# Kernel optimization log

Measured on AMD Instinct MI355X. Metric: run time of the kernel, lower is better.

Reference implementation:

```python
import jax, jax.numpy as jnp
import numpy as np

NUM_HEADS = 4
GROUPS = 8          # min(8, ch) with ch=256
EPS = 1e-5          # torch GroupNorm default eps


def setup_inputs() -> dict:
    key = jax.random.key(0)
    ks = jax.random.split(key, 3)
    b, c, h, w = 8, 256, 32, 32
    x = jax.random.normal(ks[0], (b, c, h, w), jnp.float32)
    gn_gamma = jnp.ones((c,), jnp.float32)
    gn_beta = jnp.zeros((c,), jnp.float32)
    qkv_w = jax.random.normal(ks[1], (3 * c, c), jnp.float32) * (c ** -0.5)
    qkv_b = jnp.zeros((3 * c,), jnp.float32)
    proj_w = jax.random.normal(ks[2], (c, c), jnp.float32) * (c ** -0.5)
    proj_b = jnp.zeros((c,), jnp.float32)
    return {"x": x, "gn_gamma": gn_gamma, "gn_beta": gn_beta,
            "qkv_w": qkv_w, "qkv_b": qkv_b, "proj_w": proj_w, "proj_b": proj_b}


def _group_norm(x, gamma, beta):
    b, c, h, w = x.shape
    xg = x.reshape(b, GROUPS, c // GROUPS, h, w)
    mean = xg.mean(axis=(2, 3, 4), keepdims=True)
    var = xg.var(axis=(2, 3, 4), keepdims=True)
    xn = ((xg - mean) * jax.lax.rsqrt(var + EPS)).reshape(b, c, h, w)
    return xn * gamma[None, :, None, None] + beta[None, :, None, None]


def reference(x, gn_gamma, gn_beta, qkv_w, qkv_b, proj_w, proj_b):
    b, c, h, w = x.shape
    dh = c // NUM_HEADS
    xn = _group_norm(x, gn_gamma, gn_beta)
    # 1x1 conv == channel matmul
    qkv = jnp.einsum('oc,bchw->bohw', qkv_w, xn) + qkv_b[None, :, None, None]
    qkv = qkv.reshape(b, 3, NUM_HEADS, dh, h * w)
    q, k, v = qkv[:, 0], qkv[:, 1], qkv[:, 2]   # each (b, n, dh, hw)
    scale = dh ** -0.5
    # full (hw x hw) attention matrix, matching the original explicit einsum
    attn = jax.nn.softmax(jnp.einsum('bncd,bnce->bnde', q, k) * scale, axis=-1)
    out = jnp.einsum('bnde,bnce->bncd', attn, v).reshape(b, c, h, w)
    out = jnp.einsum('oc,bchw->bohw', proj_w, out) + proj_b[None, :, None, None]
    return x + out
```

## Files before the change

### kernel.cpp

```cpp
#include <hip/hip_runtime.h>
#include <stdint.h>

typedef __attribute__((ext_vector_type(8))) short short8;
typedef __attribute__((ext_vector_type(4))) float f32x4;
typedef __attribute__((ext_vector_type(16))) float f32x16;
typedef unsigned long long u64;

#define BB 8
#define CC 256
#define PP 1024
#define NH 4
#define DH 64

#define QSCALE 0.18033688f

__device__ __forceinline__ unsigned short f2bf(float f) {
  union { float f; unsigned u; } v; v.f = f;
  unsigned r = v.u + 0x7FFFu + ((v.u >> 16) & 1u);
  return (unsigned short)(r >> 16);
}

__device__ __forceinline__ f32x4 mfma16(short8 a, short8 b, f32x4 c) {
  return __builtin_amdgcn_mfma_f32_16x16x32_bf16(a, b, c, 0, 0, 0);
}
__device__ __forceinline__ f32x16 mfma32(short8 a, short8 b, f32x16 c) {
  return __builtin_amdgcn_mfma_f32_32x32x16_bf16(a, b, c, 0, 0, 0);
}

__global__ __launch_bounds__(256) void prep(
    const float* __restrict__ x, float2* __restrict__ part,
    const float* __restrict__ qkvw, const float* __restrict__ projw,
    unsigned short* __restrict__ wall) {
  int blk = blockIdx.x;
  int tid = threadIdx.x;
  if (blk < 512) {
    int sl = blk & 7, g = (blk >> 3) & 7, b = blk >> 6;
    const float4* xb =
        (const float4*)(x + (size_t)(b * CC + g * 32) * PP) + sl * 1024;
    float s = 0.f, q = 0.f;
    for (int i = tid; i < 1024; i += 256) {
      float4 v = xb[i];
      s += v.x + v.y + v.z + v.w;
      q += v.x * v.x + v.y * v.y + v.z * v.z + v.w * v.w;
    }
    for (int off = 32; off > 0; off >>= 1) {
      s += __shfl_down(s, off);
      q += __shfl_down(q, off);
    }
    __shared__ float rs[4], rq[4];
    int w = tid >> 6;
    if ((tid & 63) == 0) { rs[w] = s; rq[w] = q; }
    __syncthreads();
    if (tid == 0)
      part[blk] = make_float2(rs[0] + rs[1] + rs[2] + rs[3],
                              rq[0] + rq[1] + rq[2] + rq[3]);
  } else {
    int i4 = (blk - 512) * 256 + tid;
    float4 v = (i4 < 49152) ? ((const float4*)qkvw)[i4]
                            : ((const float4*)projw)[i4 - 49152];
    ushort4 o;
    o.x = f2bf(v.x); o.y = f2bf(v.y); o.z = f2bf(v.z); o.w = f2bf(v.w);
    ((ushort4*)wall)[i4] = o;
  }
}

__global__ __launch_bounds__(256, 3) void nqkv(
    const float* __restrict__ x, const float2* __restrict__ part,
    const float* __restrict__ gamma, const float* __restrict__ beta,
    const unsigned short* __restrict__ wbf, const float* __restrict__ qkvb,
    unsigned short* __restrict__ qb, unsigned short* __restrict__ kb,
    unsigned short* __restrict__ vT) {
  int bid = blockIdx.x;
  int c8 = bid & 7, rr = bid >> 3;
  int t = rr % 6, base = rr / 6;
  int p0 = base * 64, b = c8, o0 = t * 128;
  int tid = threadIdx.x;
  int w = tid >> 6, lane = tid & 63, lq = lane >> 4, ln = lane & 15;
  int wy = w >> 1, wx = w & 1;
  __shared__ unsigned short A_l[64][42];
  __shared__ unsigned short B_l[128][40];
  __shared__ float scs[256], shs[256];
  __shared__ float g_m[8], g_r[8];
  if (tid < 8) {
    float S = 0.f, Q = 0.f;
    for (int i = 0; i < 8; ++i) {
      float2 pp = part[b * 64 + tid * 8 + i];
      S += pp.x; Q += pp.y;
    }
    float mean = S * (1.f / 32768.f);
    float var = Q * (1.f / 32768.f) - mean * mean;
    g_m[tid] = mean;
    g_r[tid] = rsqrtf(var + 1e-5f);
  }
  __syncthreads();
  {
    int c = tid;
    float sc = g_r[c >> 5] * gamma[c];
    scs[c] = sc;
    shs[c] = beta[c] - g_m[c >> 5] * sc;
  }
  __syncthreads();
  f32x4 acc[2][4];
  for (int i = 0; i < 2; ++i)
    for (int j = 0; j < 4; ++j) acc[i][j] = (f32x4){0.f, 0.f, 0.f, 0.f};
  int cc = tid >> 3, ps = tid & 7;
  for (int kc = 0; kc < 256; kc += 32) {
    {
      float sc = scs[kc + cc], sh = shs[kc + cc];
      const float* xr = x + ((size_t)(b * CC + kc + cc)) * PP + p0;
#pragma unroll
      for (int i = 0; i < 2; ++i) {
        int p = ps * 4 + 32 * i;
        float4 v = *(const float4*)(xr + p);
        A_l[p + 0][cc] = f2bf(v.x * sc + sh);
        A_l[p + 1][cc] = f2bf(v.y * sc + sh);
        A_l[p + 2][cc] = f2bf(v.z * sc + sh);
        A_l[p + 3][cc] = f2bf(v.w * sc + sh);
      }
    }
    for (int it = 0; it < 2; ++it) {
      int l = tid + 256 * it;
      int row = l >> 2, seg = l & 3;
      *(short8*)&B_l[row][seg * 8] =
          *(const short8*)(wbf + (size_t)(o0 + row) * CC + kc + seg * 8);
    }
    __syncthreads();
    short8 af[2], bfr[4];
    for (int i = 0; i < 2; ++i)
      af[i] = *(const short8*)&A_l[wy * 32 + i * 16 + ln][lq * 8];
    for (int j = 0; j < 4; ++j)
      bfr[j] = *(const short8*)&B_l[wx * 64 + j * 16 + ln][lq * 8];
    for (int i = 0; i < 2; ++i)
      for (int j = 0; j < 4; ++j) acc[i][j] = mfma16(af[i], bfr[j], acc[i][j]);
    __syncthreads();
  }
  for (int i = 0; i < 2; ++i) {
    for (int j = 0; j < 4; ++j) {
      int o = o0 + wx * 64 + j * 16 + ln;
      int s = o >> 8, h = (o >> 6) & 3, ch = o & 63;
      float bias = qkvb[o];
      float mul = (s == 0) ? QSCALE : 1.0f;
      size_t bh = (size_t)b * NH + h;
      int pbase = p0 + wy * 32 + i * 16 + lq * 4;
      if (s == 2) {
        union { unsigned short u[4]; u64 ll; } pk;
#pragma unroll
        for (int r = 0; r < 4; ++r) pk.u[r] = f2bf(acc[i][j][r] + bias);
        *(u64*)(vT + (bh * DH + ch) * PP + pbase) = pk.ll;
      } else {
        unsigned short* dst = (s == 0) ? qb : kb;
#pragma unroll
        for (int r = 0; r < 4; ++r)
          dst[(bh * PP + pbase + r) * DH + ch] =
              f2bf((acc[i][j][r] + bias) * mul);
      }
    }
  }
}

__global__ __launch_bounds__(256, 2) void attn(
    const unsigned short* __restrict__ qb, const unsigned short* __restrict__ kb,
    const unsigned short* __restrict__ vT, unsigned short* __restrict__ attnT) {
  int bid = blockIdx.x;
  int c8 = bid & 7, rr = bid >> 3;
  int t16 = rr & 15, base = rr >> 4;
  int g = base * 8 + c8;
  int h = g & 3, b = g >> 2;
  int d0 = t16 * 64;
  int tid = threadIdx.x;
  int w = tid >> 6, lane = tid & 63;
  int n = lane & 31, hi = lane >> 5;
  int wd = w & 1, we = w >> 1;
  size_t bh = (size_t)b * NH + h;
  const unsigned short* qbase = qb + bh * PP * DH;
  const unsigned short* kbase = kb + bh * PP * DH;
  const unsigned short* vbase = vT + bh * DH * PP;

  __shared__ __align__(16) char smem[32768];
  unsigned short* K_ls = (unsigned short*)smem;
  unsigned short* V_ls = (unsigned short*)(smem + 16384);
  float* Ored = (float*)smem;
  float* lsred = (float*)(smem + 17408);
  unsigned short* O_l = (unsigned short*)(smem + 17664);

#define KIDX(e, cb) ((e) * 64 + (((cb) ^ ((e) & 7)) << 3))
#define VIDX(ch, cb, off) ((ch) * 128 + (((cb) ^ ((ch) & 7)) << 3) + (off))

  int ke = tid >> 1, kseg = tid & 1;
  int vch = tid >> 2, vseg = tid & 3;

  short8 qf[4];
  {
    int dq = d0 + wd * 32 + n;
#pragma unroll
    for (int kc = 0; kc < 4; ++kc)
      qf[kc] = *(const short8*)(qbase + (size_t)dq * DH + kc * 16 + hi * 8);
  }
  float l_sum = 0.f;
  f32x16 o_acc[2];
#pragma unroll
  for (int i = 0; i < 16; ++i) { o_acc[0][i] = 0.f; o_acc[1][i] = 0.f; }

  short8 kr[4], vr[4];
#pragma unroll
  for (int i = 0; i < 4; ++i)
    kr[i] = *(const short8*)(kbase + (size_t)ke * DH + kseg * 32 + i * 8);
#pragma unroll
  for (int i = 0; i < 4; ++i)
    vr[i] = *(const short8*)(vbase + (size_t)vch * PP + vseg * 32 + i * 8);

  for (int e0 = 0; e0 < PP; e0 += 128) {
#pragma unroll
    for (int i = 0; i < 4; ++i)
      *(short8*)&K_ls[KIDX(ke, kseg * 4 + i)] = kr[i];
#pragma unroll
    for (int i = 0; i < 4; ++i) {
      int acb = vseg * 4 + i;
      int blkA = acb >> 1;
      int h8 = acb & 1;
      union { short8 v; u64 q[2]; } uv; uv.v = vr[i];
      *(u64*)&V_ls[VIDX(vch, blkA * 2 + 0, h8 * 4)] = uv.q[0];
      *(u64*)&V_ls[VIDX(vch, blkA * 2 + 1, h8 * 4)] = uv.q[1];
    }
    if (e0 + 128 < PP) {
      int en = e0 + 128;
#pragma unroll
      for (int i = 0; i < 4; ++i)
        kr[i] = *(const short8*)(kbase + (size_t)(en + ke) * DH + kseg * 32 + i * 8);
#pragma unroll
      for (int i = 0; i < 4; ++i)
        vr[i] = *(const short8*)(vbase + (size_t)vch * PP + en + vseg * 32 + i * 8);
    }
    __syncthreads();
    u64 pk[2][4];
#pragma unroll
    for (int t = 0; t < 2; ++t) {
      f32x16 s;
#pragma unroll
      for (int i = 0; i < 16; ++i) s[i] = 0.f;
      int erow = we * 64 + t * 32 + n;
#pragma unroll
      for (int kc = 0; kc < 4; ++kc) {
        short8 af = *(const short8*)&K_ls[KIDX(erow, kc * 2 + hi)];
        s = mfma32(af, qf[kc], s);
      }
#pragma unroll
      for (int gg = 0; gg < 4; ++gg) {
        float p0 = __builtin_amdgcn_exp2f(fminf(s[4 * gg + 0], 86.f));
        float p1 = __builtin_amdgcn_exp2f(fminf(s[4 * gg + 1], 86.f));
        float p2 = __builtin_amdgcn_exp2f(fminf(s[4 * gg + 2], 86.f));
        float p3 = __builtin_amdgcn_exp2f(fminf(s[4 * gg + 3], 86.f));
        l_sum += (p0 + p1) + (p2 + p3);
        union { unsigned short u[4]; u64 ll; } pkk;
        pkk.u[0] = f2bf(p0); pkk.u[1] = f2bf(p1);
        pkk.u[2] = f2bf(p2); pkk.u[3] = f2bf(p3);
        pk[t][gg] = pkk.ll;
      }
    }
#pragma unroll
    for (int t = 0; t < 2; ++t) {
#pragma unroll
      for (int c = 0; c < 2; ++c) {
        union { u64 q[2]; short8 v; } pf;
        pf.q[0] = pk[t][2 * c];
        pf.q[1] = pk[t][2 * c + 1];
        int cb = we * 8 + t * 4 + c * 2 + hi;
#pragma unroll
        for (int mt = 0; mt < 2; ++mt) {
          int ch = mt * 32 + n;
          short8 af = *(const short8*)&V_ls[VIDX(ch, cb, 0)];
          o_acc[mt] = mfma32(af, pf.v, o_acc[mt]);
        }
      }
    }
    __syncthreads();
  }
  l_sum += __shfl_xor(l_sum, 32);
  if (we == 1) {
    if (hi == 0) lsred[wd * 32 + n] = l_sum;
#pragma unroll
    for (int mt = 0; mt < 2; ++mt)
#pragma unroll
      for (int r = 0; r < 16; ++r) {
        int chl = (r & 3) + 8 * (r >> 2) + 4 * hi;
        Ored[(wd * 64 + mt * 32 + chl) * 34 + n] = o_acc[mt][r];
      }
  }
  __syncthreads();
  if (we == 0) {
    float inv = 1.f / (l_sum + lsred[wd * 32 + n]);
#pragma unroll
    for (int mt = 0; mt < 2; ++mt) {
#pragma unroll
      for (int gg = 0; gg < 4; ++gg) {
        union { unsigned short u[4]; u64 ll; } pkk;
#pragma unroll
        for (int q = 0; q < 4; ++q) {
          int r = gg * 4 + q;
          int chl = q + 8 * gg + 4 * hi;
          float v = (o_acc[mt][r] + Ored[(wd * 64 + mt * 32 + chl) * 34 + n]) * inv;
          pkk.u[q] = f2bf(v);
        }
        *(u64*)&O_l[(wd * 32 + n) * 72 + mt * 32 + gg * 8 + 4 * hi] = pkk.ll;
      }
    }
  }
  __syncthreads();
  for (int it = 0; it < 2; ++it) {
    int l2 = tid + 256 * it;
    int dd = l2 >> 3, seg = l2 & 7;
    *(short8*)(attnT + ((size_t)b * PP + d0 + dd) * CC + h * DH + seg * 8) =
        *(const short8*)&O_l[dd * 72 + seg * 8];
  }
#undef KIDX
#undef VIDX
}

__global__ __launch_bounds__(256) void proj_gemm(
    const unsigned short* __restrict__ attnT, const unsigned short* __restrict__ pwbf,
    const float* __restrict__ projb, const float* __restrict__ x,
    float* __restrict__ out) {
  int bid = blockIdx.x;
  int c8 = bid & 7, rr = bid >> 3;
  int t = rr & 3, base = rr >> 2;
  int p0 = base * 64, b = c8, o0 = t * 64;
  int tid = threadIdx.x;
  int w = tid >> 6, lane = tid & 63, lq = lane >> 4, ln = lane & 15;
  __shared__ unsigned short A_l[64][40];
  __shared__ unsigned short B_l[64][40];
  f32x4 acc[4];
  for (int i = 0; i < 4; ++i) acc[i] = (f32x4){0.f, 0.f, 0.f, 0.f};
  for (int kc = 0; kc < 256; kc += 32) {
    {
      int row = tid >> 2, seg = tid & 3;
      *(short8*)&A_l[row][seg * 8] =
          *(const short8*)(pwbf + (size_t)(o0 + row) * CC + kc + seg * 8);
      *(short8*)&B_l[row][seg * 8] =
          *(const short8*)(attnT + ((size_t)b * PP + p0 + row) * CC + kc + seg * 8);
    }
    __syncthreads();
    short8 af[4];
    for (int i = 0; i < 4; ++i)
      af[i] = *(const short8*)&A_l[i * 16 + ln][lq * 8];
    short8 bfr = *(const short8*)&B_l[w * 16 + ln][lq * 8];
    for (int i = 0; i < 4; ++i) acc[i] = mfma16(af[i], bfr, acc[i]);
    __syncthreads();
  }
  int p = p0 + w * 16 + ln;
  for (int i = 0; i < 4; ++i) {
    for (int r = 0; r < 4; ++r) {
      int o = o0 + i * 16 + lq * 4 + r;
      size_t idx = ((size_t)b * CC + o) * PP + p;
      out[idx] = x[idx] + projb[o] + acc[i][r];
    }
  }
}

extern "C" void kernel_launch(void* const* d_in, const int* in_sizes, int n_in,
                              void* d_out, int out_size, void* d_ws, size_t ws_size,
                              hipStream_t stream) {
  const float* x = (const float*)d_in[0];
  const float* gamma = (const float*)d_in[1];
  const float* beta = (const float*)d_in[2];
  const float* qkvw = (const float*)d_in[3];
  const float* qkvb = (const float*)d_in[4];
  const float* projw = (const float*)d_in[5];
  const float* projb = (const float*)d_in[6];
  float* out = (float*)d_out;
  char* ws = (char*)d_ws;

  float2* part = (float2*)(ws + 0);
  unsigned short* wall = (unsigned short*)(ws + 4210688);
  unsigned short* pwbf = wall + 768 * 256;
  unsigned short* qb = (unsigned short*)(ws + 4734976);
  unsigned short* kb = (unsigned short*)(ws + 8929280);
  unsigned short* vT = (unsigned short*)(ws + 13123584);
  unsigned short* attnT = (unsigned short*)(ws + 17317888);

  prep<<<768, 256, 0, stream>>>(x, part, qkvw, projw, wall);
  nqkv<<<768, 256, 0, stream>>>(x, part, gamma, beta, wall, qkvb, qb, kb, vT);
  attn<<<512, 256, 0, stream>>>(qb, kb, vT, attnT);
  proj_gemm<<<512, 256, 0, stream>>>(attnT, pwbf, projb, x, out);
}
```

Baseline: 115.0 us.

## Halve attention and projection tiles to double grid size and occupancy

The attention kernel now processes 32 query rows per block instead of 64. Its four waves each take a quarter of every 128-key chunk, and their partial outputs and row sums are combined through shared memory. The grid doubles to 1024 blocks and launch bounds request 4 blocks per CU. The projection GEMM likewise uses 32-pixel tiles with 1024 blocks. The aim is to fill the 256 CUs better, at the cost of reloading K/V twice as often in total and adding a heavier cross-wave reduction.

```diff
diff --git a/kernel.cpp b/kernel.cpp
--- a/kernel.cpp
+++ b/kernel.cpp
@@ -158,19 +158,18 @@
   }
 }
 
-__global__ __launch_bounds__(256, 2) void attn(
+__global__ __launch_bounds__(256, 4) void attn(
     const unsigned short* __restrict__ qb, const unsigned short* __restrict__ kb,
     const unsigned short* __restrict__ vT, unsigned short* __restrict__ attnT) {
   int bid = blockIdx.x;
   int c8 = bid & 7, rr = bid >> 3;
-  int t16 = rr & 15, base = rr >> 4;
+  int t32 = rr & 31, base = rr >> 5;
   int g = base * 8 + c8;
   int h = g & 3, b = g >> 2;
-  int d0 = t16 * 64;
+  int d0 = t32 * 32;
   int tid = threadIdx.x;
-  int w = tid >> 6, lane = tid & 63;
+  int we = tid >> 6, lane = tid & 63;
   int n = lane & 31, hi = lane >> 5;
-  int wd = w & 1, we = w >> 1;
   size_t bh = (size_t)b * NH + h;
   const unsigned short* qbase = qb + bh * PP * DH;
   const unsigned short* kbase = kb + bh * PP * DH;
@@ -180,8 +179,8 @@
   unsigned short* K_ls = (unsigned short*)smem;
   unsigned short* V_ls = (unsigned short*)(smem + 16384);
   float* Ored = (float*)smem;
-  float* lsred = (float*)(smem + 17408);
-  unsigned short* O_l = (unsigned short*)(smem + 17664);
+  float* lsred = (float*)(smem + 25344);
+  unsigned short* O_l = (unsigned short*)(smem + 25728);
 
 #define KIDX(e, cb) ((e) * 64 + (((cb) ^ ((e) & 7)) << 3))
 #define VIDX(ch, cb, off) ((ch) * 128 + (((cb) ^ ((ch) & 7)) << 3) + (off))
@@ -191,7 +190,7 @@
 
   short8 qf[4];
   {
-    int dq = d0 + wd * 32 + n;
+    int dq = d0 + n;
 #pragma unroll
     for (int kc = 0; kc < 4; ++kc)
       qf[kc] = *(const short8*)(qbase + (size_t)dq * DH + kc * 16 + hi * 8);
@@ -232,13 +231,12 @@
         vr[i] = *(const short8*)(vbase + (size_t)vch * PP + en + vseg * 32 + i * 8);
     }
     __syncthreads();
-    u64 pk[2][4];
-#pragma unroll
-    for (int t = 0; t < 2; ++t) {
+    u64 pk[4];
+    {
       f32x16 s;
 #pragma unroll
       for (int i = 0; i < 16; ++i) s[i] = 0.f;
-      int erow = we * 64 + t * 32 + n;
+      int erow = we * 32 + n;
 #pragma unroll
       for (int kc = 0; kc < 4; ++kc) {
         short8 af = *(const short8*)&K_ls[KIDX(erow, kc * 2 + hi)];
@@ -254,41 +252,38 @@
         union { unsigned short u[4]; u64 ll; } pkk;
         pkk.u[0] = f2bf(p0); pkk.u[1] = f2bf(p1);
         pkk.u[2] = f2bf(p2); pkk.u[3] = f2bf(p3);
-        pk[t][gg] = pkk.ll;
-      }
-    }
-#pragma unroll
-    for (int t = 0; t < 2; ++t) {
-#pragma unroll
-      for (int c = 0; c < 2; ++c) {
-        union { u64 q[2]; short8 v; } pf;
-        pf.q[0] = pk[t][2 * c];
-        pf.q[1] = pk[t][2 * c + 1];
-        int cb = we * 8 + t * 4 + c * 2 + hi;
-#pragma unroll
-        for (int mt = 0; mt < 2; ++mt) {
-          int ch = mt * 32 + n;
-          short8 af = *(const short8*)&V_ls[VIDX(ch, cb, 0)];
-          o_acc[mt] = mfma32(af, pf.v, o_acc[mt]);
-        }
+        pk[gg] = pkk.ll;
+      }
+    }
+#pragma unroll
+    for (int c = 0; c < 2; ++c) {
+      union { u64 q[2]; short8 v; } pf;
+      pf.q[0] = pk[2 * c];
+      pf.q[1] = pk[2 * c + 1];
+      int cb = we * 4 + c * 2 + hi;
+#pragma unroll
+      for (int mt = 0; mt < 2; ++mt) {
+        int ch = mt * 32 + n;
+        short8 af = *(const short8*)&V_ls[VIDX(ch, cb, 0)];
+        o_acc[mt] = mfma32(af, pf.v, o_acc[mt]);
       }
     }
     __syncthreads();
   }
   l_sum += __shfl_xor(l_sum, 32);
-  if (we == 1) {
-    if (hi == 0) lsred[wd * 32 + n] = l_sum;
+  if (we != 0) {
+    if (hi == 0) lsred[(we - 1) * 32 + n] = l_sum;
 #pragma unroll
     for (int mt = 0; mt < 2; ++mt)
 #pragma unroll
       for (int r = 0; r < 16; ++r) {
         int chl = (r & 3) + 8 * (r >> 2) + 4 * hi;
-        Ored[(wd * 64 + mt * 32 + chl) * 34 + n] = o_acc[mt][r];
+        Ored[((we - 1) * 64 + mt * 32 + chl) * 33 + n] = o_acc[mt][r];
       }
   }
   __syncthreads();
   if (we == 0) {
-    float inv = 1.f / (l_sum + lsred[wd * 32 + n]);
+    float inv = 1.f / (l_sum + lsred[n] + lsred[32 + n] + lsred[64 + n]);
 #pragma unroll
     for (int mt = 0; mt < 2; ++mt) {
 #pragma unroll
@@ -298,17 +293,18 @@
         for (int q = 0; q < 4; ++q) {
           int r = gg * 4 + q;
           int chl = q + 8 * gg + 4 * hi;
-          float v = (o_acc[mt][r] + Ored[(wd * 64 + mt * 32 + chl) * 34 + n]) * inv;
-          pkk.u[q] = f2bf(v);
+          float v = o_acc[mt][r] + Ored[(mt * 32 + chl) * 33 + n] +
+                    Ored[(64 + mt * 32 + chl) * 33 + n] +
+                    Ored[(128 + mt * 32 + chl) * 33 + n];
+          pkk.u[q] = f2bf(v * inv);
         }
-        *(u64*)&O_l[(wd * 32 + n) * 72 + mt * 32 + gg * 8 + 4 * hi] = pkk.ll;
+        *(u64*)&O_l[n * 72 + mt * 32 + gg * 8 + 4 * hi] = pkk.ll;
       }
     }
   }
   __syncthreads();
-  for (int it = 0; it < 2; ++it) {
-    int l2 = tid + 256 * it;
-    int dd = l2 >> 3, seg = l2 & 7;
+  {
+    int dd = tid >> 3, seg = tid & 7;
     *(short8*)(attnT + ((size_t)b * PP + d0 + dd) * CC + h * DH + seg * 8) =
         *(const short8*)&O_l[dd * 72 + seg * 8];
   }
@@ -323,33 +319,35 @@
   int bid = blockIdx.x;
   int c8 = bid & 7, rr = bid >> 3;
   int t = rr & 3, base = rr >> 2;
-  int p0 = base * 64, b = c8, o0 = t * 64;
+  int p0 = base * 32, b = c8, o0 = t * 64;
   int tid = threadIdx.x;
   int w = tid >> 6, lane = tid & 63, lq = lane >> 4, ln = lane & 15;
+  int wo = w >> 1, wp = w & 1;
   __shared__ unsigned short A_l[64][40];
-  __shared__ unsigned short B_l[64][40];
-  f32x4 acc[4];
-  for (int i = 0; i < 4; ++i) acc[i] = (f32x4){0.f, 0.f, 0.f, 0.f};
+  __shared__ unsigned short B_l[32][40];
+  f32x4 acc[2];
+  for (int i = 0; i < 2; ++i) acc[i] = (f32x4){0.f, 0.f, 0.f, 0.f};
   for (int kc = 0; kc < 256; kc += 32) {
     {
       int row = tid >> 2, seg = tid & 3;
       *(short8*)&A_l[row][seg * 8] =
           *(const short8*)(pwbf + (size_t)(o0 + row) * CC + kc + seg * 8);
-      *(short8*)&B_l[row][seg * 8] =
-          *(const short8*)(attnT + ((size_t)b * PP + p0 + row) * CC + kc + seg * 8);
-    }
-    __syncthreads();
-    short8 af[4];
-    for (int i = 0; i < 4; ++i)
-      af[i] = *(const short8*)&A_l[i * 16 + ln][lq * 8];
-    short8 bfr = *(const short8*)&B_l[w * 16 + ln][lq * 8];
-    for (int i = 0; i < 4; ++i) acc[i] = mfma16(af[i], bfr, acc[i]);
-    __syncthreads();
-  }
-  int p = p0 + w * 16 + ln;
-  for (int i = 0; i < 4; ++i) {
+      if (tid < 128)
+        *(short8*)&B_l[row][seg * 8] =
+            *(const short8*)(attnT + ((size_t)b * PP + p0 + row) * CC + kc + seg * 8);
+    }
+    __syncthreads();
+    short8 af[2];
+    for (int i = 0; i < 2; ++i)
+      af[i] = *(const short8*)&A_l[wo * 32 + i * 16 + ln][lq * 8];
+    short8 bfr = *(const short8*)&B_l[wp * 16 + ln][lq * 8];
+    for (int i = 0; i < 2; ++i) acc[i] = mfma16(af[i], bfr, acc[i]);
+    __syncthreads();
+  }
+  int p = p0 + wp * 16 + ln;
+  for (int i = 0; i < 2; ++i) {
     for (int r = 0; r < 4; ++r) {
-      int o = o0 + i * 16 + lq * 4 + r;
+      int o = o0 + wo * 32 + i * 16 + lq * 4 + r;
       size_t idx = ((size_t)b * CC + o) * PP + p;
       out[idx] = x[idx] + projb[o] + acc[i][r];
     }
@@ -379,6 +377,6 @@
 
   prep<<<768, 256, 0, stream>>>(x, part, qkvw, projw, wall);
   nqkv<<<768, 256, 0, stream>>>(x, part, gamma, beta, wall, qkvb, qb, kb, vT);
-  attn<<<512, 256, 0, stream>>>(qb, kb, vT, attnT);
-  proj_gemm<<<512, 256, 0, stream>>>(attnT, pwbf, projb, x, out);
-}
+  attn<<<1024, 256, 0, stream>>>(qb, kb, vT, attnT);
+  proj_gemm<<<1024, 256, 0, stream>>>(attnT, pwbf, projb, x, out);
+}
```

New measurement: 120.1 us. 1.04x slower.
